# Kernel optimization log

Hardware: AMD Instinct MI355X
Metric: run time of the kernel (lower is better)

## Reference

```python
import jax, jax.numpy as jnp
import numpy as np

N_NODES = 100000
N_EDGES = 3200000
IN_F = 512
HID = 256
SAMPLE = 32768
EPS = 1e-5  # BatchNorm1d default eps


def _xavier(k, shape):
    lim = np.sqrt(6.0 / (shape[0] + shape[1]))
    return jax.random.uniform(k, shape, jnp.float32, -lim, lim)


def setup_inputs() -> dict:
    key = jax.random.key(0)
    ks = jax.random.split(key, 6)
    x = jax.random.normal(ks[0], (N_NODES, IN_F), jnp.float32)
    edge_index = jax.random.randint(ks[1], (2, N_EDGES), 0, N_NODES, dtype=jnp.int32)
    W1 = _xavier(ks[2], (IN_F, HID)); b1 = jnp.zeros((HID,), jnp.float32)
    W2 = _xavier(ks[3], (HID, HID)); b2 = jnp.zeros((HID,), jnp.float32)
    W3 = _xavier(ks[4], (HID, 1));   b3 = jnp.zeros((1,), jnp.float32)
    gamma1 = jnp.ones((HID,), jnp.float32); beta1 = jnp.zeros((HID,), jnp.float32)
    gamma2 = jnp.ones((HID,), jnp.float32); beta2 = jnp.zeros((HID,), jnp.float32)
    return dict(x=x, edge_index=edge_index, W1=W1, b1=b1, W2=W2, b2=b2,
                W3=W3, b3=b3, gamma1=gamma1, beta1=beta1, gamma2=gamma2, beta2=beta2)


def _batchnorm(h, gamma, beta):
    # training-mode BN: batch mean, biased variance (matches torch forward)
    mu = h.mean(axis=0)
    var = h.var(axis=0)
    return gamma * (h - mu) / jnp.sqrt(var + EPS) + beta


def _conv(h, row, col, valid, W, b):
    support = h @ W                              # [S, out]
    msg = support[row] * valid[:, None]          # gather + edge-weight mask
    out = jax.ops.segment_sum(msg, col, num_segments=SAMPLE)  # scatter_add
    return out + b


def reference(x, edge_index, W1, b1, W2, b2, W3, b3, gamma1, beta1, gamma2, beta2):
    skey = jax.random.key(42)
    # fastgcn_sampler: degree-proportional sampling with replacement
    deg = jax.ops.segment_sum(jnp.ones((N_EDGES,), jnp.float32), edge_index[0],
                              num_segments=N_NODES)
    sampled = jax.random.choice(skey, N_NODES, (SAMPLE,), replace=True, p=deg / deg.sum())
    mapping = jax.ops.segment_max(jnp.arange(SAMPLE, dtype=jnp.int32), sampled,
                                  num_segments=N_NODES)
    row_m = mapping[edge_index[0]]
    col_m = mapping[edge_index[1]]
    ok = (row_m >= 0) & (col_m >= 0)             # edge kept iff both endpoints sampled
    valid = ok.astype(x.dtype)
    row = jnp.where(ok, row_m, 0)
    col = jnp.where(ok, col_m, 0)
    xs = x[sampled]                              # [S, IN_F] irregular gather
    h = _conv(xs, row, col, valid, W1, b1)
    h = jax.nn.relu(_batchnorm(h, gamma1, beta1))  # dropout off (eval determinism)
    h = _conv(h, row, col, valid, W2, b2)
    h = jax.nn.relu(_batchnorm(h, gamma2, beta2))
    out = _conv(h, row, col, valid, W3, b3)      # [S, 1]
    return out, sampled
```

## Files before the change

kernel.cpp:

```cpp
#include <hip/hip_runtime.h>
#include <stdint.h>
#include <stddef.h>

#define NNODES 100000
#define NEDGES 3200000
#define INFEAT 512
#define HID 256
#define SMP 32768
#define BNEPS 1e-5f

__device__ __forceinline__ uint32_t rotl32(uint32_t x, int d) { return (x << d) | (x >> (32 - d)); }

__device__ __forceinline__ void threefry2x32(uint32_t k0, uint32_t k1, uint32_t& x0, uint32_t& x1) {
  const uint32_t ks0 = k0, ks1 = k1, ks2 = k0 ^ k1 ^ 0x1BD11BDAu;
  x0 += ks0; x1 += ks1;
#define TFR(r) { x0 += x1; x1 = rotl32(x1, r); x1 ^= x0; }
  TFR(13) TFR(15) TFR(26) TFR(6)
  x0 += ks1; x1 += ks2 + 1u;
  TFR(17) TFR(29) TFR(16) TFR(24)
  x0 += ks2; x1 += ks0 + 2u;
  TFR(13) TFR(15) TFR(26) TFR(6)
  x0 += ks0; x1 += ks1 + 3u;
  TFR(17) TFR(29) TFR(16) TFR(24)
  x0 += ks1; x1 += ks2 + 4u;
  TFR(13) TFR(15) TFR(26) TFR(6)
  x0 += ks2; x1 += ks0 + 5u;
#undef TFR
}

__global__ __launch_bounds__(256) void k_deg(const int* __restrict__ erow, int* __restrict__ deg) {
  int i = blockIdx.x * 256 + threadIdx.x;
  if (i < NEDGES) atomicAdd(&deg[erow[i]], 1);
}

__global__ __launch_bounds__(256) void k_down(const int* __restrict__ deg, float* __restrict__ E) {
  __shared__ float l0[4096];
  __shared__ float l1[2048];
  const int t = threadIdx.x;
  const int base0 = blockIdx.x * 4096;
  const int n0 = min(4096, NNODES - base0);
  for (int i = t; i < n0; i += 256) {
    float p = (float)deg[base0 + i] / 3200000.0f;
    l0[i] = p;
    E[base0 + i] = p;
  }
  __syncthreads();
  const int b1 = base0 >> 1, n1 = min(2048, 50000 - b1);
  for (int k = t; k < n1; k += 256) { float v = l0[2*k] + l0[2*k+1]; l1[k] = v; E[100000 + b1 + k] = v; }
  __syncthreads();
  const int b2 = base0 >> 2, n2 = min(1024, 25000 - b2);
  for (int k = t; k < n2; k += 256) { float v = l1[2*k] + l1[2*k+1]; l0[k] = v; E[150000 + b2 + k] = v; }
  __syncthreads();
  const int b3 = base0 >> 3, n3 = min(512, 12500 - b3);
  for (int k = t; k < n3; k += 256) { float v = l0[2*k] + l0[2*k+1]; l1[k] = v; E[175000 + b3 + k] = v; }
  __syncthreads();
  const int b4 = base0 >> 4, n4 = min(256, 6250 - b4);
  for (int k = t; k < n4; k += 256) { float v = l1[2*k] + l1[2*k+1]; E[187500 + b4 + k] = v; }
}

__device__ __constant__ int kMidN[12] = {3125,1562,781,390,195,97,48,24,12,6,3,1};
__device__ __constant__ int kMidO[12] = {0,3125,4687,5468,5858,6053,6150,6198,6222,6234,6240,6243};
__global__ __launch_bounds__(1024) void k_mid(const float* __restrict__ E, float* __restrict__ CS) {
  __shared__ float eb[6244];
  __shared__ float sb[6244];
  const int t = threadIdx.x;
  const float* e4 = E + 187500;
  for (int k = t; k < 3125; k += 1024) eb[k] = e4[2*k] + e4[2*k+1];
  __syncthreads();
  for (int li = 1; li < 12; ++li) {
    const float* src = eb + kMidO[li-1];
    float* dst = eb + kMidO[li];
    const int n = kMidN[li];
    for (int k = t; k < n; k += 1024) dst[k] = src[2*k] + src[2*k+1];
    __syncthreads();
  }
  if (t == 0) sb[6243] = eb[6243];
  __syncthreads();
  for (int li = 10; li >= 0; --li) {
    const float* el = eb + kMidO[li];
    const float* sh = sb + kMidO[li+1];
    float* sl = sb + kMidO[li];
    const int n = kMidN[li], nh = kMidN[li+1];
    for (int k = t; k < nh; k += 1024) {
      float v = sh[k];
      sl[2*k+1] = v;
      if (2*k+2 < n) sl[2*k+2] = v + el[2*k+2];
    }
    if (t == 0) sl[0] = el[0];
    __syncthreads();
  }
  for (int k = t; k < 3125; k += 1024) CS[193750 + k] = sb[k];
}

__global__ __launch_bounds__(256) void k_up(const float* __restrict__ sh, const float* __restrict__ el,
                                            float* __restrict__ sl, int n) {
  int j = blockIdx.x * 256 + threadIdx.x;
  if (j >= n) return;
  if (j == 0) { sl[0] = el[0]; return; }
  float v = sh[(j - 1) >> 1];
  sl[j] = (j & 1) ? v : v + el[j];
}

__global__ __launch_bounds__(256) void k_sample(const float* __restrict__ cum, int* __restrict__ sampled,
                                                int* __restrict__ mapping, float* __restrict__ outSamp) {
  int i = blockIdx.x * 256 + threadIdx.x;
  if (i >= SMP) return;
  uint32_t x0 = 0u, x1 = (uint32_t)i;
  threefry2x32(0u, 42u, x0, x1);
  uint32_t bits = x0 ^ x1;
  float u = __uint_as_float((bits >> 9) | 0x3f800000u) - 1.0f;
  float r = cum[NNODES - 1] * (1.0f - u);
  int lo = 0, hi = NNODES;
  while (lo < hi) {
    int mid = (lo + hi) >> 1;
    if (cum[mid] < r) lo = mid + 1; else hi = mid;
  }
  if (lo > NNODES - 1) lo = NNODES - 1;
  sampled[i] = lo;
  outSamp[i] = (float)lo;
  atomicMax(&mapping[lo], i);
}

__global__ __launch_bounds__(256) void k_edge_count(const int* __restrict__ erow, const int* __restrict__ ecol,
                                                    const int* __restrict__ mapping, int* __restrict__ cnt) {
  int i = blockIdx.x * 256 + threadIdx.x;
  if (i >= NEDGES) return;
  int r = mapping[erow[i]];
  int c = mapping[ecol[i]];
  if ((r | c) >= 0) atomicAdd(&cnt[c], 1);
}

__global__ __launch_bounds__(1024) void k_scan(const int* __restrict__ cnt, int* __restrict__ rowptr,
                                               int* __restrict__ cursor) {
  __shared__ int tot[1024];
  const int t = threadIdx.x;
  const int base = t * 32;
  int local[32];
  int s = 0;
#pragma unroll
  for (int i = 0; i < 32; ++i) { local[i] = s; s += cnt[base + i]; }
  tot[t] = s;
  __syncthreads();
  for (int o = 1; o < 1024; o <<= 1) {
    int v = (t >= o) ? tot[t - o] : 0;
    __syncthreads();
    tot[t] += v;
    __syncthreads();
  }
  int excl = (t == 0) ? 0 : tot[t - 1];
#pragma unroll
  for (int i = 0; i < 32; ++i) {
    int v = excl + local[i];
    rowptr[base + i] = v;
    cursor[base + i] = v;
  }
  if (t == 1023) rowptr[SMP] = tot[1023];
}

__global__ __launch_bounds__(256) void k_edge_fill(const int* __restrict__ erow, const int* __restrict__ ecol,
                                                   const int* __restrict__ mapping, int* __restrict__ cursor,
                                                   int* __restrict__ srcidx) {
  int i = blockIdx.x * 256 + threadIdx.x;
  if (i >= NEDGES) return;
  int r = mapping[erow[i]];
  int c = mapping[ecol[i]];
  if ((r | c) < 0) return;
  int pos = atomicAdd(&cursor[c], 1);
  srcidx[pos] = r;
}

__global__ __launch_bounds__(256) void k_segsum(const float* __restrict__ S, const int* __restrict__ rowptr,
                                                const int* __restrict__ srcidx, float* __restrict__ A) {
  const int wave = threadIdx.x >> 6, lane = threadIdx.x & 63;
  const int c = blockIdx.x * 4 + wave;
  const int b = rowptr[c], e = rowptr[c + 1];
  float4 acc = make_float4(0.f, 0.f, 0.f, 0.f);
  for (int i = b; i < e; ++i) {
    int r = srcidx[i];
    float4 v = *(const float4*)(S + (size_t)r * HID + lane * 4);
    acc.x += v.x; acc.y += v.y; acc.z += v.z; acc.w += v.w;
  }
  *(float4*)(A + (size_t)c * HID + lane * 4) = acc;
}

__global__ __launch_bounds__(256) void k_segsum_sc(const float* __restrict__ s3, const int* __restrict__ rowptr,
                                                   const int* __restrict__ srcidx, const float* __restrict__ b3,
                                                   float* __restrict__ out) {
  int c = blockIdx.x * 256 + threadIdx.x;
  if (c >= SMP) return;
  float acc = 0.f;
  const int e = rowptr[c + 1];
  for (int i = rowptr[c]; i < e; ++i) acc += s3[srcidx[i]];
  out[c] = acc + b3[0];
}

__global__ __launch_bounds__(256) void k_gemm(const float* __restrict__ Am, const float* __restrict__ Bm,
                                              float* __restrict__ Cm, const int* __restrict__ gather, int K) {
  __shared__ float As[16][68];
  __shared__ float Bs[16][64];
  const int t = threadIdx.x;
  const int tx = t & 15, ty = t >> 4;
  const int row0 = blockIdx.x * 64, col0 = blockIdx.y * 64;
  const int ar = t >> 2, ak = (t & 3) << 2;
  int arow = row0 + ar;
  if (gather) arow = gather[arow];
  const float* aptr = Am + (size_t)arow * K + ak;
  const int kb = t >> 4, cb = (t & 15) << 2;
  const float* bptr = Bm + (size_t)kb * HID + col0 + cb;
  float acc[4][4] = {};
  for (int k0 = 0; k0 < K; k0 += 16) {
    float4 av = *(const float4*)(aptr + k0);
    float4 bv = *(const float4*)(bptr + (size_t)k0 * HID);
    As[ak + 0][ar] = av.x;
    As[ak + 1][ar] = av.y;
    As[ak + 2][ar] = av.z;
    As[ak + 3][ar] = av.w;
    *(float4*)&Bs[kb][cb] = bv;
    __syncthreads();
#pragma unroll
    for (int kk = 0; kk < 16; ++kk) {
      float4 a = *(const float4*)&As[kk][ty << 2];
      float4 b = *(const float4*)&Bs[kk][tx << 2];
      acc[0][0] = fmaf(a.x, b.x, acc[0][0]); acc[0][1] = fmaf(a.x, b.y, acc[0][1]);
      acc[0][2] = fmaf(a.x, b.z, acc[0][2]); acc[0][3] = fmaf(a.x, b.w, acc[0][3]);
      acc[1][0] = fmaf(a.y, b.x, acc[1][0]); acc[1][1] = fmaf(a.y, b.y, acc[1][1]);
      acc[1][2] = fmaf(a.y, b.z, acc[1][2]); acc[1][3] = fmaf(a.y, b.w, acc[1][3]);
      acc[2][0] = fmaf(a.z, b.x, acc[2][0]); acc[2][1] = fmaf(a.z, b.y, acc[2][1]);
      acc[2][2] = fmaf(a.z, b.z, acc[2][2]); acc[2][3] = fmaf(a.z, b.w, acc[2][3]);
      acc[3][0] = fmaf(a.w, b.x, acc[3][0]); acc[3][1] = fmaf(a.w, b.y, acc[3][1]);
      acc[3][2] = fmaf(a.w, b.z, acc[3][2]); acc[3][3] = fmaf(a.w, b.w, acc[3][3]);
    }
    __syncthreads();
  }
#pragma unroll
  for (int i = 0; i < 4; ++i) {
    float4 v = make_float4(acc[i][0], acc[i][1], acc[i][2], acc[i][3]);
    *(float4*)(Cm + (size_t)(row0 + (ty << 2) + i) * HID + col0 + (tx << 2)) = v;
  }
}

__global__ __launch_bounds__(256) void k_bn_stats(const float* __restrict__ A, const float* __restrict__ bias,
                                                  float* __restrict__ sums, float* __restrict__ sumsq) {
  const int c = threadIdx.x;
  const float b = bias[c];
  float s = 0.f, q = 0.f;
  const int r0 = blockIdx.x * (SMP / 256);
  for (int r = r0; r < r0 + (SMP / 256); ++r) {
    float h = A[(size_t)r * HID + c] + b;
    s += h;
    q = fmaf(h, h, q);
  }
  unsafeAtomicAdd(&sums[c], s);
  unsafeAtomicAdd(&sumsq[c], q);
}

__global__ __launch_bounds__(256) void k_bn_final(const float* __restrict__ sums, const float* __restrict__ sumsq,
    const float* __restrict__ gamma, const float* __restrict__ beta,
    float* __restrict__ scale, float* __restrict__ shift) {
  int c = threadIdx.x;
  float mu = sums[c] * (1.0f / SMP);
  float var = fmaxf(sumsq[c] * (1.0f / SMP) - mu * mu, 0.0f);
  float sc = gamma[c] / sqrtf(var + BNEPS);
  scale[c] = sc;
  shift[c] = beta[c] - mu * sc;
}

__global__ __launch_bounds__(256) void k_bn_apply(const float* __restrict__ A, const float* __restrict__ bias,
    const float* __restrict__ scale, const float* __restrict__ shift, float* __restrict__ Hh) {
  const int total = SMP * HID / 4;
  for (int i = blockIdx.x * 256 + threadIdx.x; i < total; i += gridDim.x * 256) {
    int c = (i & (HID / 4 - 1)) * 4;
    float4 v = ((const float4*)A)[i];
    v.x = fmaxf(fmaf(v.x + bias[c + 0], scale[c + 0], shift[c + 0]), 0.f);
    v.y = fmaxf(fmaf(v.y + bias[c + 1], scale[c + 1], shift[c + 1]), 0.f);
    v.z = fmaxf(fmaf(v.z + bias[c + 2], scale[c + 2], shift[c + 2]), 0.f);
    v.w = fmaxf(fmaf(v.w + bias[c + 3], scale[c + 3], shift[c + 3]), 0.f);
    ((float4*)Hh)[i] = v;
  }
}

__global__ __launch_bounds__(256) void k_gemv3(const float* __restrict__ Hh, const float* __restrict__ W3,
                                               float* __restrict__ s3) {
  const int wave = threadIdx.x >> 6, lane = threadIdx.x & 63;
  const int row = blockIdx.x * 4 + wave;
  float4 h = *(const float4*)(Hh + (size_t)row * HID + lane * 4);
  float4 w = *(const float4*)(W3 + lane * 4);
  float d = h.x * w.x + h.y * w.y + h.z * w.z + h.w * w.w;
#pragma unroll
  for (int o = 32; o > 0; o >>= 1) d += __shfl_down(d, o);
  if (lane == 0) s3[row] = d;
}

extern "C" void kernel_launch(void* const* d_in, const int* in_sizes, int n_in,
                              void* d_out, int out_size, void* d_ws, size_t ws_size,
                              hipStream_t stream) {
  (void)in_sizes; (void)n_in; (void)out_size; (void)ws_size;
  const float* x   = (const float*)d_in[0];
  const int*  eidx = (const int*)d_in[1];
  const float* W1  = (const float*)d_in[2];
  const float* b1  = (const float*)d_in[3];
  const float* W2  = (const float*)d_in[4];
  const float* b2  = (const float*)d_in[5];
  const float* W3  = (const float*)d_in[6];
  const float* b3  = (const float*)d_in[7];
  const float* g1  = (const float*)d_in[8];
  const float* be1 = (const float*)d_in[9];
  const float* g2  = (const float*)d_in[10];
  const float* be2 = (const float*)d_in[11];
  const int* erow = eidx;
  const int* ecol = eidx + NEDGES;

  float* out = (float*)d_out;
  float* outSamp = out + SMP;

  size_t off = 0;
  auto take = [&](size_t bytes) -> char* {
    char* p = (char*)d_ws + off;
    off += (bytes + 255) & ~(size_t)255;
    return p;
  };
  float* S       = (float*)take((size_t)SMP * HID * 4);
  float* A       = (float*)take((size_t)SMP * HID * 4);
  float* H       = (float*)take((size_t)SMP * HID * 4);
  float* E       = (float*)take(199994 * 4);
  float* CS      = (float*)take(199994 * 4);
  int*   deg     = (int*)take(NNODES * 4);
  int*   mapping = (int*)take(NNODES * 4);
  int*   sampled = (int*)take(SMP * 4);
  float* sums    = (float*)take(HID * 4 * 2);
  float* sumsq   = sums + HID;
  float* scale   = (float*)take(HID * 4);
  float* shift   = (float*)take(HID * 4);
  int*   cnt     = (int*)take(SMP * 4);
  int*   rowptr  = (int*)take((SMP + 1) * 4);
  int*   cursor  = (int*)take(SMP * 4);
  int*   srcidx  = (int*)take((size_t)NEDGES * 4);

  hipMemsetAsync(deg, 0, NNODES * 4, stream);
  hipMemsetAsync(mapping, 0xFF, NNODES * 4, stream);
  hipMemsetAsync(cnt, 0, SMP * 4, stream);

  k_deg<<<(NEDGES + 255) / 256, 256, 0, stream>>>(erow, deg);

  k_down<<<25, 256, 0, stream>>>(deg, E);
  k_mid<<<1, 1024, 0, stream>>>(E, CS);
  k_up<<<(6250 + 255) / 256, 256, 0, stream>>>(CS + 193750, E + 187500, CS + 187500, 6250);
  k_up<<<(12500 + 255) / 256, 256, 0, stream>>>(CS + 187500, E + 175000, CS + 175000, 12500);
  k_up<<<(25000 + 255) / 256, 256, 0, stream>>>(CS + 175000, E + 150000, CS + 150000, 25000);
  k_up<<<(50000 + 255) / 256, 256, 0, stream>>>(CS + 150000, E + 100000, CS + 100000, 50000);
  k_up<<<(100000 + 255) / 256, 256, 0, stream>>>(CS + 100000, E, CS, 100000);

  k_sample<<<SMP / 256, 256, 0, stream>>>(CS, sampled, mapping, outSamp);

  k_edge_count<<<(NEDGES + 255) / 256, 256, 0, stream>>>(erow, ecol, mapping, cnt);
  k_scan<<<1, 1024, 0, stream>>>(cnt, rowptr, cursor);
  k_edge_fill<<<(NEDGES + 255) / 256, 256, 0, stream>>>(erow, ecol, mapping, cursor, srcidx);

  k_gemm<<<dim3(SMP / 64, HID / 64), 256, 0, stream>>>(x, W1, S, sampled, INFEAT);
  k_segsum<<<SMP / 4, 256, 0, stream>>>(S, rowptr, srcidx, A);
  hipMemsetAsync(sums, 0, HID * 4 * 2, stream);
  k_bn_stats<<<256, 256, 0, stream>>>(A, b1, sums, sumsq);
  k_bn_final<<<1, HID, 0, stream>>>(sums, sumsq, g1, be1, scale, shift);
  k_bn_apply<<<2048, 256, 0, stream>>>(A, b1, scale, shift, H);

  k_gemm<<<dim3(SMP / 64, HID / 64), 256, 0, stream>>>(H, W2, S, nullptr, HID);
  k_segsum<<<SMP / 4, 256, 0, stream>>>(S, rowptr, srcidx, A);
  hipMemsetAsync(sums, 0, HID * 4 * 2, stream);
  k_bn_stats<<<256, 256, 0, stream>>>(A, b2, sums, sumsq);
  k_bn_final<<<1, HID, 0, stream>>>(sums, sumsq, g2, be2, scale, shift);
  k_bn_apply<<<2048, 256, 0, stream>>>(A, b2, scale, shift, H);

  k_gemv3<<<SMP / 4, 256, 0, stream>>>(H, W3, S);
  k_segsum_sc<<<SMP / 256, 256, 0, stream>>>(S, rowptr, srcidx, b3, out);
}
```

Before: 800.0 us.

## Replace global atomic degree histogram with two-pass bucket partition and LDS counting

The single kernel that did one global atomicAdd per edge to count node degrees is replaced by two passes. The first pass partitions each 4096-edge chunk by node bucket (512 nodes per bucket) in shared memory and records per-chunk bucket offsets. The second pass has one block per bucket accumulate counts in a shared-memory histogram and write deg directly, so the memset is no longer needed. This trades global atomic contention for an extra full read and write of the edge array, and the count kernel runs only 196 blocks, each thread looping serially over its segments.

```diff
diff --git a/kernel.cpp b/kernel.cpp
--- a/kernel.cpp
+++ b/kernel.cpp
@@ -8,6 +8,11 @@
 #define HID 256
 #define SMP 32768
 #define BNEPS 1e-5f
+
+#define PA_EPB 4096
+#define PA_BLOCKS ((NEDGES + PA_EPB - 1) / PA_EPB)
+#define NBUCK 196
+#define BBITS 9
 
 __device__ __forceinline__ uint32_t rotl32(uint32_t x, int d) { return (x << d) | (x >> (32 - d)); }
 
@@ -28,9 +33,69 @@
 #undef TFR
 }
 
-__global__ __launch_bounds__(256) void k_deg(const int* __restrict__ erow, int* __restrict__ deg) {
-  int i = blockIdx.x * 256 + threadIdx.x;
-  if (i < NEDGES) atomicAdd(&deg[erow[i]], 1);
+__global__ __launch_bounds__(256) void k_part(const int* __restrict__ erow,
+                                              int* __restrict__ part, int* __restrict__ lbaseg) {
+  __shared__ int hist[NBUCK];
+  __shared__ int cnt2[NBUCK];
+  __shared__ int base[NBUCK];
+  __shared__ int sc[256];
+  __shared__ int staged[PA_EPB];
+  const int t = threadIdx.x;
+  const int s = blockIdx.x;
+  const int e0 = s * PA_EPB;
+  const int n = min(PA_EPB, NEDGES - e0);
+  for (int i = t; i < NBUCK; i += 256) { hist[i] = 0; cnt2[i] = 0; }
+  __syncthreads();
+  int nodes[16];
+  int cnt = 0;
+  for (int i = t; i < n; i += 256) nodes[cnt++] = erow[e0 + i];
+  for (int j = 0; j < cnt; ++j) atomicAdd(&hist[nodes[j] >> BBITS], 1);
+  __syncthreads();
+  sc[t] = (t < NBUCK) ? hist[t] : 0;
+  __syncthreads();
+  for (int o = 1; o < 256; o <<= 1) {
+    int v = (t >= o) ? sc[t - o] : 0;
+    __syncthreads();
+    sc[t] += v;
+    __syncthreads();
+  }
+  if (t < NBUCK) {
+    base[t] = sc[t] - hist[t];
+    lbaseg[s * NBUCK + t] = base[t];
+  }
+  __syncthreads();
+  for (int j = 0; j < cnt; ++j) {
+    int b = nodes[j] >> BBITS;
+    int r = atomicAdd(&cnt2[b], 1);
+    staged[base[b] + r] = nodes[j];
+  }
+  __syncthreads();
+  for (int i = t; i < n; i += 256) part[e0 + i] = staged[i];
+}
+
+__global__ __launch_bounds__(256) void k_count(const int* __restrict__ part,
+                                               const int* __restrict__ lbaseg, int* __restrict__ deg) {
+  __shared__ int hist[512];
+  const int t = threadIdx.x;
+  const int b = blockIdx.x;
+  for (int i = t; i < 512; i += 256) hist[i] = 0;
+  __syncthreads();
+  for (int s = t; s < PA_BLOCKS; s += 256) {
+    const int e0 = s * PA_EPB;
+    const int n = min(PA_EPB, NEDGES - e0);
+    const int st = lbaseg[s * NBUCK + b];
+    const int en = (b < NBUCK - 1) ? lbaseg[s * NBUCK + b + 1] : n;
+    for (int i = st; i < en; ++i) {
+      int node = part[e0 + i];
+      atomicAdd(&hist[node & 511], 1);
+    }
+  }
+  __syncthreads();
+  const int n0 = b << BBITS;
+  for (int i = t; i < 512; i += 256) {
+    int idx = n0 + i;
+    if (idx < NNODES) deg[idx] = hist[i];
+  }
 }
 
 __global__ __launch_bounds__(256) void k_down(const int* __restrict__ deg, float* __restrict__ E) {
@@ -325,6 +390,8 @@
   float* E       = (float*)take(199994 * 4);
   float* CS      = (float*)take(199994 * 4);
   int*   deg     = (int*)take(NNODES * 4);
+  int*   part    = (int*)take((size_t)NEDGES * 4);
+  int*   lbaseg  = (int*)take((size_t)PA_BLOCKS * NBUCK * 4);
   int*   mapping = (int*)take(NNODES * 4);
   int*   sampled = (int*)take(SMP * 4);
   float* sums    = (float*)take(HID * 4 * 2);
@@ -336,11 +403,11 @@
   int*   cursor  = (int*)take(SMP * 4);
   int*   srcidx  = (int*)take((size_t)NEDGES * 4);
 
-  hipMemsetAsync(deg, 0, NNODES * 4, stream);
   hipMemsetAsync(mapping, 0xFF, NNODES * 4, stream);
   hipMemsetAsync(cnt, 0, SMP * 4, stream);
 
-  k_deg<<<(NEDGES + 255) / 256, 256, 0, stream>>>(erow, deg);
+  k_part<<<PA_BLOCKS, 256, 0, stream>>>(erow, part, lbaseg);
+  k_count<<<NBUCK, 256, 0, stream>>>(part, lbaseg, deg);
 
   k_down<<<25, 256, 0, stream>>>(deg, E);
   k_mid<<<1, 1024, 0, stream>>>(E, CS);
```

Measured after the change: 727.0 us. 9.1% less time.
